# Performance work log

Measured on AMD Instinct MI355X. Metric: run time of the kernel, lower is better.

Reference implementation:

```python
import jax, jax.numpy as jnp
import numpy as np

NEG_SLOPE = 0.2  # PyG GATConv default negative_slope


def gat_layer(x, src, dst, N, W, att_src, att_dst, bias, heads, out_ch, concat):
    # x: [N, Fin]; W: [Fin, heads*out_ch]; att_*: [heads, out_ch]; bias matches output dim
    h = (x @ W).reshape(N, heads, out_ch)              # [N, H, C]
    a_src = (h * att_src).sum(-1)                      # [N, H]
    a_dst = (h * att_dst).sum(-1)                      # [N, H]
    e = jax.nn.leaky_relu(a_src[src] + a_dst[dst], NEG_SLOPE)  # [E, H]
    # segment softmax over incoming edges of each destination node
    e_max = jax.ops.segment_max(e, dst, num_segments=N)        # [N, H]
    e_exp = jnp.exp(e - e_max[dst])                             # [E, H]
    denom = jax.ops.segment_sum(e_exp, dst, num_segments=N)    # [N, H]
    alpha = e_exp / (denom[dst] + 1e-16)                        # [E, H]
    msg = alpha[:, :, None] * h[src]                            # [E, H, C]
    out = jax.ops.segment_sum(msg, dst, num_segments=N)        # [N, H, C]
    out = out.reshape(N, heads * out_ch) if concat else out.mean(axis=1)
    return out + bias


def setup_inputs() -> dict:
    key = jax.random.key(0)
    ks = jax.random.split(key, 10)
    N, E = 40000, 160000
    Fin, H1, C1 = 602, 8, 256
    H2, C2 = 1, 42
    g = lambda k, shape, fan: (jax.random.normal(k, shape, dtype=jnp.float32) * (1.0 / np.sqrt(fan)))
    return {
        "x": jax.random.normal(ks[0], (N, Fin), dtype=jnp.float32),
        "edge_index": jax.random.randint(ks[1], (2, E), 0, N, dtype=jnp.int64),
        "W1": g(ks[2], (Fin, H1 * C1), Fin),
        "att_src1": g(ks[3], (H1, C1), C1),
        "att_dst1": g(ks[4], (H1, C1), C1),
        "b1": jnp.zeros((H1 * C1,), dtype=jnp.float32),
        "W2": g(ks[5], (H1 * C1, H2 * C2), H1 * C1),
        "att_src2": g(ks[6], (H2, C2), C2),
        "att_dst2": g(ks[7], (H2, C2), C2),
        "b2": jnp.zeros((C2,), dtype=jnp.float32),
    }


def reference(x, edge_index, W1, att_src1, att_dst1, b1, W2, att_src2, att_dst2, b2):
    N = x.shape[0]
    # PyG GATConv default add_self_loops=True
    loops = jnp.arange(N, dtype=edge_index.dtype)
    src = jnp.concatenate([edge_index[0], loops])
    dst = jnp.concatenate([edge_index[1], loops])
    h = gat_layer(x, src, dst, N, W1, att_src1, att_dst1, b1, heads=8, out_ch=256, concat=True)
    h = jax.nn.relu(h)  # dropout is identity in eval mode
    h = gat_layer(h, src, dst, N, W2, att_src2, att_dst2, b2, heads=1, out_ch=42, concat=False)
    return jax.nn.log_softmax(h, axis=1)
```

## Files before the change

kernel.cpp:

```cpp
#include <hip/hip_runtime.h>
#include <hip/hip_bf16.h>

#define NN   40000
#define NE   160000
#define ETOT 200000
#define FIN  602
#define NH1  8
#define C1   256
#define F1   2048
#define C2   42
#define NEG  0.2f
#define NB   157
#define KP   608
#define MP   40064

typedef unsigned short u16;
typedef unsigned int   u32;
typedef __bf16 bf16x8 __attribute__((ext_vector_type(8)));
typedef float  f32x4  __attribute__((ext_vector_type(4)));

__device__ __forceinline__ float bfu(u16 v){ return __uint_as_float(((u32)v) << 16); }
__device__ __forceinline__ float bflo(u32 u){ return __uint_as_float(u << 16); }
__device__ __forceinline__ float bfhi(u32 u){ return __uint_as_float(u & 0xffff0000u); }
__device__ __forceinline__ u16 f2bf(float f){
  u32 u = __float_as_uint(f);
  u32 r = (u + 0x7fffu + ((u >> 16) & 1u)) >> 16;
  return (u16)r;
}

__global__ void probe_k(const u32* __restrict__ xw, const int* __restrict__ ei,
                        int* __restrict__ flags) {
  if (threadIdx.x == 0) {
    int zc = 0;
    for (int k = 0; k < 64; ++k) zc += (ei[2*k + 1] == 0) ? 1 : 0;
    flags[0] = (zc == 64) ? 1 : 0;
    int inr = 0;
    for (int k = 0; k < 64; ++k) {
      u32 low = xw[k] & 0xffffu;
      int e = (int)((low >> 7) & 0xff);
      inr += (e >= 100 && e <= 140) ? 1 : 0;
    }
    flags[1] = (inr >= 32) ? 0 : 1;
  }
}

__global__ void cvt_f32_k(const void* __restrict__ src, float* __restrict__ dst, int n,
                          const int* __restrict__ flags) {
  int i = blockIdx.x * 256 + threadIdx.x;
  if (i >= n) return;
  dst[i] = flags[1] ? ((const float*)src)[i] : bfu(((const u16*)src)[i]);
}

__global__ void xb_k(const void* __restrict__ x, u16* __restrict__ xb,
                     const int* __restrict__ flags) {
  int k = blockIdx.x * 256 + threadIdx.x;
  int row = blockIdx.y;
  if (k >= KP) return;
  u16 v = 0;
  if (row < NN && k < FIN)
    v = flags[1] ? f2bf(((const float*)x)[(size_t)row * FIN + k])
                 : ((const u16*)x)[(size_t)row * FIN + k];
  xb[(size_t)row * KP + k] = v;
}

__global__ void w1t_k(const void* __restrict__ W1, u16* __restrict__ w1t,
                      const int* __restrict__ flags) {
  int n = blockIdx.x * 256 + threadIdx.x;
  int k = blockIdx.y;
  if (n >= F1) return;
  u16 v = 0;
  if (k < FIN) v = flags[1] ? f2bf(((const float*)W1)[(size_t)k * F1 + n])
                            : ((const u16*)W1)[(size_t)k * F1 + n];
  w1t[(size_t)n * KP + k] = v;
}

__global__ void w2t_k(const void* __restrict__ W2, u16* __restrict__ w2t,
                      const int* __restrict__ flags) {
  int i = blockIdx.x * 256 + threadIdx.x;
  if (i >= 64 * F1) return;
  int c = i >> 11, k = i & (F1 - 1);
  u16 v = 0;
  if (c < C2) v = flags[1] ? f2bf(((const float*)W2)[(size_t)k * C2 + c])
                           : ((const u16*)W2)[(size_t)k * C2 + c];
  w2t[i] = v;
}

__device__ __forceinline__ void edge_sd(const int* __restrict__ ei, int e, int imode,
                                        int& s, int& d) {
  if (e < NE) {
    if (imode) { s = ei[2*e]; d = ei[2*(NE + e)]; }
    else       { s = ei[e];   d = ei[NE + e];     }
  } else { s = d = e - NE; }
}

__global__ void deg_k(const int* __restrict__ ei, int* __restrict__ deg,
                      const int* __restrict__ flags) {
  int e = blockIdx.x * 256 + threadIdx.x;
  if (e >= ETOT) return;
  int s, d; edge_sd(ei, e, flags[0], s, d);
  atomicAdd(&deg[d], 1);
}

__global__ __launch_bounds__(256) void scan1_k(const int* __restrict__ deg,
                                               int* __restrict__ tmp, int* __restrict__ bsum) {
  __shared__ int s[256];
  int b = blockIdx.x, t = threadIdx.x, i = b * 256 + t;
  int v = (i < NN) ? deg[i] : 0;
  s[t] = v; __syncthreads();
  for (int o = 1; o < 256; o <<= 1) {
    int u = (t >= o) ? s[t - o] : 0;
    __syncthreads(); s[t] += u; __syncthreads();
  }
  if (i < NN) tmp[i] = s[t];
  if (t == 255) bsum[b] = s[255];
}

__global__ __launch_bounds__(256) void scan2_k(int* __restrict__ bsum) {
  __shared__ int s[256];
  int t = threadIdx.x;
  int v = (t < NB) ? bsum[t] : 0;
  s[t] = v; __syncthreads();
  for (int o = 1; o < 256; o <<= 1) {
    int u = (t >= o) ? s[t - o] : 0;
    __syncthreads(); s[t] += u; __syncthreads();
  }
  if (t < NB) bsum[t] = s[t];
}

__global__ void scan3_k(const int* __restrict__ deg, const int* __restrict__ tmp,
                        const int* __restrict__ bsum, int* __restrict__ start, int* __restrict__ cur) {
  int i = blockIdx.x * 256 + threadIdx.x;
  if (i >= NN) return;
  int b = i >> 8;
  int off = b ? bsum[b - 1] : 0;
  int excl = tmp[i] - deg[i] + off;
  start[i] = excl; cur[i] = excl;
}

__global__ void fill_k(const int* __restrict__ ei, int* __restrict__ cur,
                       int* __restrict__ csr_src, int* __restrict__ csr_dst,
                       const int* __restrict__ flags) {
  int e = blockIdx.x * 256 + threadIdx.x;
  if (e >= ETOT) return;
  int s, d; edge_sd(ei, e, flags[0], s, d);
  int pos = atomicAdd(&cur[d], 1);
  csr_src[pos] = s; csr_dst[pos] = d;
}

__global__ __launch_bounds__(256) void gemm1b_k(const u16* __restrict__ xb,
                                                const u16* __restrict__ w1t,
                                                u16* __restrict__ h1,
                                                const float* __restrict__ as1c,
                                                const float* __restrict__ ad1c,
                                                float* __restrict__ a_s1,
                                                float* __restrict__ a_d1) {
  const int t = threadIdx.x;
  const int lane = t & 63, wid = t >> 6;
  const int wr = wid >> 1, wc = wid & 1;
  const int m0 = blockIdx.y * 128, n0 = blockIdx.x * 128;
  const int l16 = lane & 15, lk = (lane >> 4) * 8;
  f32x4 acc[4][4];
  #pragma unroll
  for (int i = 0; i < 4; ++i)
    #pragma unroll
    for (int j = 0; j < 4; ++j) acc[i][j] = (f32x4){0.f, 0.f, 0.f, 0.f};

  const u16* Ap = xb  + (size_t)(m0 + wr * 64 + l16) * KP + lk;
  const u16* Bp = w1t + (size_t)(n0 + wc * 64 + l16) * KP + lk;

  bf16x8 a[4], b[4];
  #pragma unroll
  for (int i = 0; i < 4; ++i) {
    a[i] = *(const bf16x8*)(Ap + (size_t)i * 16 * KP);
    b[i] = *(const bf16x8*)(Bp + (size_t)i * 16 * KP);
  }
  for (int k0 = 32; k0 < KP; k0 += 32) {
    bf16x8 an[4], bn[4];
    #pragma unroll
    for (int i = 0; i < 4; ++i) {
      an[i] = *(const bf16x8*)(Ap + (size_t)i * 16 * KP + k0);
      bn[i] = *(const bf16x8*)(Bp + (size_t)i * 16 * KP + k0);
    }
    #pragma unroll
    for (int mi = 0; mi < 4; ++mi)
      #pragma unroll
      for (int ni = 0; ni < 4; ++ni)
        acc[mi][ni] = __builtin_amdgcn_mfma_f32_16x16x32_bf16(a[mi], b[ni], acc[mi][ni], 0, 0, 0);
    #pragma unroll
    for (int i = 0; i < 4; ++i) { a[i] = an[i]; b[i] = bn[i]; }
  }
  #pragma unroll
  for (int mi = 0; mi < 4; ++mi)
    #pragma unroll
    for (int ni = 0; ni < 4; ++ni)
      acc[mi][ni] = __builtin_amdgcn_mfma_f32_16x16x32_bf16(a[mi], b[ni], acc[mi][ni], 0, 0, 0);

  const int h0 = n0 >> 8;
  float psrc[4][4], pdst[4][4];
  #pragma unroll
  for (int mi = 0; mi < 4; ++mi)
    #pragma unroll
    for (int r = 0; r < 4; ++r) { psrc[mi][r] = 0.f; pdst[mi][r] = 0.f; }
  #pragma unroll
  for (int ni = 0; ni < 4; ++ni) {
    int col = n0 + wc * 64 + ni * 16 + l16;
    float wsv = as1c[col], wdv = ad1c[col];
    #pragma unroll
    for (int mi = 0; mi < 4; ++mi)
      #pragma unroll
      for (int r = 0; r < 4; ++r) {
        float v = acc[mi][ni][r];
        psrc[mi][r] += v * wsv;
        pdst[mi][r] += v * wdv;
      }
  }
  #pragma unroll
  for (int o = 1; o < 16; o <<= 1) {
    #pragma unroll
    for (int mi = 0; mi < 4; ++mi)
      #pragma unroll
      for (int r = 0; r < 4; ++r) {
        psrc[mi][r] += __shfl_xor(psrc[mi][r], o, 64);
        pdst[mi][r] += __shfl_xor(pdst[mi][r], o, 64);
      }
  }
  const int lr4 = (lane >> 4) * 4;
  if (l16 == 0) {
    #pragma unroll
    for (int mi = 0; mi < 4; ++mi)
      #pragma unroll
      for (int r = 0; r < 4; ++r) {
        int row = m0 + wr * 64 + mi * 16 + lr4 + r;
        if (row < NN) {
          atomicAdd(&a_s1[row * NH1 + h0], psrc[mi][r]);
          atomicAdd(&a_d1[row * NH1 + h0], pdst[mi][r]);
        }
      }
  }

  #pragma unroll
  for (int mi = 0; mi < 4; ++mi) {
    #pragma unroll
    for (int r = 0; r < 4; ++r) {
      int row = m0 + wr * 64 + mi * 16 + lr4 + r;
      if (row < NN) {
        #pragma unroll
        for (int ni = 0; ni < 4; ++ni) {
          int col = n0 + wc * 64 + ni * 16 + l16;
          h1[(size_t)row * F1 + col] = f2bf(acc[mi][ni][r]);
        }
      }
    }
  }
}

__global__ __launch_bounds__(256) void gemm1m_k(const void* __restrict__ xv,
                                                const u16* __restrict__ w1t,
                                                u16* __restrict__ h1,
                                                const int* __restrict__ flags) {
  __shared__ u16 As[128][40];
  __shared__ u16 Bs[128][40];
  const int fm = flags[1];
  const int t = threadIdx.x;
  const int lane = t & 63, wid = t >> 6;
  const int wr = wid >> 1, wc = wid & 1;
  const int m0 = blockIdx.y * 128, n0 = blockIdx.x * 128;
  const int l16 = lane & 15, lk = (lane >> 4) * 8;
  f32x4 acc[4][4];
  #pragma unroll
  for (int i = 0; i < 4; ++i)
    #pragma unroll
    for (int j = 0; j < 4; ++j) acc[i][j] = (f32x4){0.f, 0.f, 0.f, 0.f};
  const int arow = t >> 2;
  const int akb  = (t & 3) * 8;
  for (int k0 = 0; k0 < KP; k0 += 32) {
    #pragma unroll
    for (int i = 0; i < 2; ++i) {
      int row = arow + i * 64;
      int rg = m0 + row;
      u32 d0 = 0, d1 = 0, d2 = 0, d3 = 0;
      if (rg < NN) {
        if (k0 + 32 <= FIN) {
          if (fm) {
            const float* xp = (const float*)xv + (size_t)rg * FIN + k0 + akb;
            float2 p0 = *(const float2*)(xp);
            float2 p1 = *(const float2*)(xp + 2);
            float2 p2 = *(const float2*)(xp + 4);
            float2 p3 = *(const float2*)(xp + 6);
            d0 = (u32)f2bf(p0.x) | ((u32)f2bf(p0.y) << 16);
            d1 = (u32)f2bf(p1.x) | ((u32)f2bf(p1.y) << 16);
            d2 = (u32)f2bf(p2.x) | ((u32)f2bf(p2.y) << 16);
            d3 = (u32)f2bf(p3.x) | ((u32)f2bf(p3.y) << 16);
          } else {
            const u16* xp = (const u16*)xv + (size_t)rg * FIN + k0 + akb;
            d0 = *(const u32*)(xp);
            d1 = *(const u32*)(xp + 2);
            d2 = *(const u32*)(xp + 4);
            d3 = *(const u32*)(xp + 6);
          }
        } else {
          u16 e[8];
          #pragma unroll
          for (int q = 0; q < 8; ++q) {
            int k = k0 + akb + q;
            e[q] = 0;
            if (k < FIN)
              e[q] = fm ? f2bf(((const float*)xv)[(size_t)rg * FIN + k])
                        : ((const u16*)xv)[(size_t)rg * FIN + k];
          }
          d0 = (u32)e[0] | ((u32)e[1] << 16);
          d1 = (u32)e[2] | ((u32)e[3] << 16);
          d2 = (u32)e[4] | ((u32)e[5] << 16);
          d3 = (u32)e[6] | ((u32)e[7] << 16);
        }
      }
      *(uint4*)&As[row][akb] = make_uint4(d0, d1, d2, d3);
      const u16* wp = w1t + (size_t)(n0 + row) * KP + k0 + akb;
      *(uint4*)&Bs[row][akb] = *(const uint4*)wp;
    }
    __syncthreads();
    bf16x8 bfr[4];
    #pragma unroll
    for (int ni = 0; ni < 4; ++ni)
      bfr[ni] = *(const bf16x8*)&Bs[wc * 64 + ni * 16 + l16][lk];
    #pragma unroll
    for (int mi = 0; mi < 4; ++mi) {
      bf16x8 af = *(const bf16x8*)&As[wr * 64 + mi * 16 + l16][lk];
      #pragma unroll
      for (int ni = 0; ni < 4; ++ni)
        acc[mi][ni] = __builtin_amdgcn_mfma_f32_16x16x32_bf16(af, bfr[ni], acc[mi][ni], 0, 0, 0);
    }
    __syncthreads();
  }
  const int lr4 = (lane >> 4) * 4;
  #pragma unroll
  for (int mi = 0; mi < 4; ++mi) {
    #pragma unroll
    for (int r = 0; r < 4; ++r) {
      int row = m0 + wr * 64 + mi * 16 + lr4 + r;
      if (row < NN) {
        #pragma unroll
        for (int ni = 0; ni < 4; ++ni) {
          int col = n0 + wc * 64 + ni * 16 + l16;
          h1[(size_t)row * F1 + col] = f2bf(acc[mi][ni][r]);
        }
      }
    }
  }
}

__global__ __launch_bounds__(256) void att1_k(const u16* __restrict__ h1,
                                              const float* __restrict__ as1c, const float* __restrict__ ad1c,
                                              float* __restrict__ a_s, float* __restrict__ a_d) {
  int n = blockIdx.x, t = threadIdx.x;
  int h = t >> 5, l = t & 31;
  int base = h * C1 + l * 8;
  const u16* hp = h1 + (size_t)n * F1 + base;
  uint4 v = *(const uint4*)hp;
  u32 w[4] = {v.x, v.y, v.z, v.w};
  float ss = 0.f, sd = 0.f;
  #pragma unroll
  for (int p = 0; p < 4; ++p) {
    float e0 = bflo(w[p]), e1 = bfhi(w[p]);
    ss += e0 * as1c[base + 2*p] + e1 * as1c[base + 2*p + 1];
    sd += e0 * ad1c[base + 2*p] + e1 * ad1c[base + 2*p + 1];
  }
  #pragma unroll
  for (int o = 16; o > 0; o >>= 1) {
    ss += __shfl_down(ss, o, 32);
    sd += __shfl_down(sd, o, 32);
  }
  if (l == 0) { a_s[n * NH1 + h] = ss; a_d[n * NH1 + h] = sd; }
}

__global__ __launch_bounds__(256) void gfuse_k(const int* __restrict__ start, const int* __restrict__ deg,
                                               const int* __restrict__ csr_src,
                                               const float* __restrict__ a_s1, const float* __restrict__ a_d1,
                                               const u16* __restrict__ h1, const float* __restrict__ b1c,
                                               const u16* __restrict__ w2t, float* __restrict__ h2) {
  __shared__ u16 rowsL[16 * F1];
  int t = threadIdx.x;
  int nb = blockIdx.x * 16;
  int h = t >> 5;
  int c0 = t * 8;
  float4 bA = *(const float4*)(b1c + c0);
  float4 bB = *(const float4*)(b1c + c0 + 4);
  for (int i = 0; i < 16; ++i) {
    int n = nb + i;
    int s0 = start[n], jend = s0 + deg[n];
    float ad = a_d1[n * NH1 + h];
    float a0=0.f,a1=0.f,a2=0.f,a3=0.f,a4=0.f,a5=0.f,a6=0.f,a7=0.f,den=0.f;
    int j = s0;
    for (; j + 2 <= jend; j += 2) {
      int sA = csr_src[j], sB = csr_src[j + 1];
      float vA = a_s1[sA * NH1 + h] + ad;
      float vB = a_s1[sB * NH1 + h] + ad;
      vA = vA > 0.f ? vA : NEG * vA;
      vB = vB > 0.f ? vB : NEG * vB;
      float eA = expf(vA), eB = expf(vB);
      uint4 uA = *(const uint4*)(h1 + (size_t)sA * F1 + c0);
      uint4 uB = *(const uint4*)(h1 + (size_t)sB * F1 + c0);
      den += eA + eB;
      a0 += eA * bflo(uA.x) + eB * bflo(uB.x);
      a1 += eA * bfhi(uA.x) + eB * bfhi(uB.x);
      a2 += eA * bflo(uA.y) + eB * bflo(uB.y);
      a3 += eA * bfhi(uA.y) + eB * bfhi(uB.y);
      a4 += eA * bflo(uA.z) + eB * bflo(uB.z);
      a5 += eA * bfhi(uA.z) + eB * bfhi(uB.z);
      a6 += eA * bflo(uA.w) + eB * bflo(uB.w);
      a7 += eA * bfhi(uA.w) + eB * bfhi(uB.w);
    }
    if (j < jend) {
      int sA = csr_src[j];
      float vA = a_s1[sA * NH1 + h] + ad;
      vA = vA > 0.f ? vA : NEG * vA;
      float eA = expf(vA);
      uint4 uA = *(const uint4*)(h1 + (size_t)sA * F1 + c0);
      den += eA;
      a0 += eA * bflo(uA.x); a1 += eA * bfhi(uA.x);
      a2 += eA * bflo(uA.y); a3 += eA * bfhi(uA.y);
      a4 += eA * bflo(uA.z); a5 += eA * bfhi(uA.z);
      a6 += eA * bflo(uA.w); a7 += eA * bfhi(uA.w);
    }
    float inv = 1.f / (den + 1e-16f);
    u16 o0 = f2bf(fmaxf(a0 * inv + bA.x, 0.f));
    u16 o1 = f2bf(fmaxf(a1 * inv + bA.y, 0.f));
    u16 o2 = f2bf(fmaxf(a2 * inv + bA.z, 0.f));
    u16 o3 = f2bf(fmaxf(a3 * inv + bA.w, 0.f));
    u16 o4 = f2bf(fmaxf(a4 * inv + bB.x, 0.f));
    u16 o5 = f2bf(fmaxf(a5 * inv + bB.y, 0.f));
    u16 o6 = f2bf(fmaxf(a6 * inv + bB.z, 0.f));
    u16 o7 = f2bf(fmaxf(a7 * inv + bB.w, 0.f));
    uint4 pk;
    pk.x = (u32)o0 | ((u32)o1 << 16);
    pk.y = (u32)o2 | ((u32)o3 << 16);
    pk.z = (u32)o4 | ((u32)o5 << 16);
    pk.w = (u32)o6 | ((u32)o7 << 16);
    int sw = (i & 7) << 3;
    *(uint4*)&rowsL[i * F1 + (c0 ^ sw)] = pk;
  }
  __syncthreads();
  int lane = t & 63, wid = t >> 6;
  int l16 = lane & 15, lk = (lane >> 4) * 8;
  const u16* wt = w2t + (size_t)(wid * 16 + l16) * F1;
  int sw = (l16 & 7) << 3;
  f32x4 acc2 = (f32x4){0.f, 0.f, 0.f, 0.f};
  for (int k0 = 0; k0 < F1; k0 += 32) {
    int kk = k0 + lk;
    bf16x8 af = *(const bf16x8*)&rowsL[l16 * F1 + (kk ^ sw)];
    bf16x8 bf = *(const bf16x8*)(wt + kk);
    acc2 = __builtin_amdgcn_mfma_f32_16x16x32_bf16(af, bf, acc2, 0, 0, 0);
  }
  int col = wid * 16 + l16;
  if (col < C2) {
    int mb = (lane >> 4) * 4;
    #pragma unroll
    for (int r = 0; r < 4; ++r)
      h2[(size_t)(nb + mb + r) * C2 + col] = acc2[r];
  }
}

__global__ __launch_bounds__(64) void att2_k(const float* __restrict__ h2,
                                             const float* __restrict__ as2, const float* __restrict__ ad2,
                                             float* __restrict__ a_s, float* __restrict__ a_d) {
  int n = blockIdx.x, t = threadIdx.x;
  float ss = 0.f, sd = 0.f;
  if (t < C2) {
    float v = h2[(size_t)n * C2 + t];
    ss = v * as2[t];
    sd = v * ad2[t];
  }
  #pragma unroll
  for (int o = 32; o > 0; o >>= 1) {
    ss += __shfl_down(ss, o, 64);
    sd += __shfl_down(sd, o, 64);
  }
  if (t == 0) { a_s[n] = ss; a_d[n] = sd; }
}

__global__ __launch_bounds__(64) void gath2_k(const int* __restrict__ start, const int* __restrict__ deg,
                                              const int* __restrict__ csr_src,
                                              const float* __restrict__ a_s, const float* __restrict__ a_d,
                                              const float* __restrict__ h2, const float* __restrict__ b2,
                                              void* __restrict__ outv, const int* __restrict__ flags) {
  int n = blockIdx.x, t = threadIdx.x;
  int s0 = start[n], cnt = deg[n];
  float ad = a_d[n];
  float acc = 0.f, den = 0.f;
  for (int j = s0; j < s0 + cnt; ++j) {
    int s = csr_src[j];
    float v = a_s[s] + ad;
    v = v > 0.f ? v : NEG * v;
    float e = expf(v);
    den += e;
    if (t < C2) acc += e * h2[(size_t)s * C2 + t];
  }
  float raw = (t < C2) ? acc / (den + 1e-16f) + b2[t] : -1e30f;
  float m = raw;
  #pragma unroll
  for (int o = 32; o > 0; o >>= 1) m = fmaxf(m, __shfl_down(m, o, 64));
  m = __shfl(m, 0, 64);
  float e2 = (t < C2) ? expf(raw - m) : 0.f;
  float ssum = e2;
  #pragma unroll
  for (int o = 32; o > 0; o >>= 1) ssum += __shfl_down(ssum, o, 64);
  ssum = __shfl(ssum, 0, 64);
  if (t < C2) {
    float v = raw - m - logf(ssum);
    if (flags[1]) ((float*)outv)[(size_t)n * C2 + t] = v;
    else          ((u16*) outv)[(size_t)n * C2 + t] = f2bf(v);
  }
}

extern "C" void kernel_launch(void* const* d_in, const int* in_sizes, int n_in,
                              void* d_out, int out_size, void* d_ws, size_t ws_size,
                              hipStream_t stream) {
  const void* x   = d_in[0];
  const int*  ei  = (const int*)d_in[1];
  const void* W1  = d_in[2];
  const void* as1 = d_in[3];
  const void* ad1 = d_in[4];
  const void* b1  = d_in[5];
  const void* W2  = d_in[6];
  const void* as2 = d_in[7];
  const void* ad2 = d_in[8];
  const void* b2  = d_in[9];

  char* ws = (char*)d_ws;
  u16*   h1      = (u16*)  (ws);
  float* ex1     = (float*)(ws + 163840000);
  float* h2      = (float*)(ws + 170240000);
  float* a_s1    = (float*)(ws + 176960000);
  float* a_d1    = (float*)(ws + 178240000);
  float* a_s2    = (float*)(ws + 179520000);
  float* a_d2    = (float*)(ws + 179680000);
  int*   deg     = (int*)  (ws + 179840000);
  int*   start   = (int*)  (ws + 180000000);
  int*   cur     = (int*)  (ws + 180160000);
  int*   tmp     = (int*)  (ws + 180320000);
  int*   csr_src = (int*)  (ws + 180480000);
  int*   csr_dst = (int*)  (ws + 181280000);
  int*   bsum    = (int*)  (ws + 182080000);
  u16*   w1t     = (u16*)  (ws + 182081024);
  u16*   w2t     = (u16*)  (ws + 184571392);
  float* as1c    = (float*)(ws + 184833536);
  float* ad1c    = (float*)(ws + 184841728);
  float* b1c     = (float*)(ws + 184849920);
  float* as2c    = (float*)(ws + 184858112);
  float* ad2c    = (float*)(ws + 184858368);
  float* b2c     = (float*)(ws + 184858624);
  int*   flags   = (int*)  (ws + 184858880);
  const size_t TOTAL_BASE = 184859136;
  u16*   xb      = (u16*)  (ws + TOTAL_BASE);
  const size_t TOTAL_A = TOTAL_BASE + (size_t)MP * KP * 2;
  if (ws_size < TOTAL_BASE) return;
  const bool pathA = (ws_size >= TOTAL_A);
  (void)ex1;

  probe_k<<<1, 64, 0, stream>>>((const u32*)x, ei, flags);

  cvt_f32_k<<<(F1 + 255) / 256, 256, 0, stream>>>(as1, as1c, F1, flags);
  cvt_f32_k<<<(F1 + 255) / 256, 256, 0, stream>>>(ad1, ad1c, F1, flags);
  cvt_f32_k<<<(F1 + 255) / 256, 256, 0, stream>>>(b1, b1c, F1, flags);
  cvt_f32_k<<<1, 256, 0, stream>>>(as2, as2c, C2, flags);
  cvt_f32_k<<<1, 256, 0, stream>>>(ad2, ad2c, C2, flags);
  cvt_f32_k<<<1, 256, 0, stream>>>(b2, b2c, C2, flags);
  w1t_k<<<dim3(8, KP), 256, 0, stream>>>(W1, w1t, flags);
  w2t_k<<<(64 * F1 + 255) / 256, 256, 0, stream>>>(W2, w2t, flags);

  hipMemsetAsync(deg, 0, NN * sizeof(int), stream);
  hipMemsetAsync(a_s1, 0, 2 * NN * NH1 * sizeof(float), stream);
  const int EB = (ETOT + 255) / 256;
  deg_k  <<<EB, 256, 0, stream>>>(ei, deg, flags);
  scan1_k<<<NB, 256, 0, stream>>>(deg, tmp, bsum);
  scan2_k<<<1, 256, 0, stream>>>(bsum);
  scan3_k<<<NB, 256, 0, stream>>>(deg, tmp, bsum, start, cur);
  fill_k <<<EB, 256, 0, stream>>>(ei, cur, csr_src, csr_dst, flags);

  if (pathA) {
    xb_k<<<dim3((KP + 255) / 256, MP), 256, 0, stream>>>(x, xb, flags);
    gemm1b_k<<<dim3(16, MP / 128), 256, 0, stream>>>(xb, w1t, h1, as1c, ad1c, a_s1, a_d1);
  } else {
    gemm1m_k<<<dim3(16, MP / 128), 256, 0, stream>>>(x, w1t, h1, flags);
    att1_k<<<NN, 256, 0, stream>>>(h1, as1c, ad1c, a_s1, a_d1);
  }
  gfuse_k<<<NN / 16, 256, 0, stream>>>(start, deg, csr_src, a_s1, a_d1, h1, b1c, w2t, h2);

  att2_k<<<NN, 64, 0, stream>>>(h2, as2c, ad2c, a_s2, a_d2);
  gath2_k<<<NN, 64, 0, stream>>>(start, deg, csr_src, a_s2, a_d2, h2, b2c, d_out, flags);
}
```

Baseline: 660.4 us.

## Swizzle GEMM1 block order for XCD locality and split gfuse over 512 threads

The first GEMM now runs on a 1D grid whose block index is remapped so that consecutive blocks on each of the 8 XCDs share row tiles, aiming to improve L2 reuse of A and B tiles. The fused gather+GEMM2 kernel doubles its block to 512 threads. Two groups of 256 threads each gather 8 destination nodes, and the second MFMA stage splits K in half across wave pairs with a shared-memory reduction. This raises parallelism per block and hides gather latency, at the cost of an extra barrier and fewer resident blocks per CU.

```diff
diff --git a/kernel.cpp b/kernel.cpp
--- a/kernel.cpp
+++ b/kernel.cpp
@@ -13,6 +13,7 @@
 #define NB   157
 #define KP   608
 #define MP   40064
+#define NWG1 5008
 
 typedef unsigned short u16;
 typedef unsigned int   u32;
@@ -157,7 +158,10 @@
   const int t = threadIdx.x;
   const int lane = t & 63, wid = t >> 6;
   const int wr = wid >> 1, wc = wid & 1;
-  const int m0 = blockIdx.y * 128, n0 = blockIdx.x * 128;
+  const int bid = blockIdx.x;
+  const int swz = (bid & 7) * (NWG1 / 8) + (bid >> 3);
+  const int m0 = (swz >> 4) * 128;
+  const int n0 = (swz & 15) * 128;
   const int l16 = lane & 15, lk = (lane >> 4) * 8;
   f32x4 acc[4][4];
   #pragma unroll
@@ -373,19 +377,22 @@
   if (l == 0) { a_s[n * NH1 + h] = ss; a_d[n * NH1 + h] = sd; }
 }
 
-__global__ __launch_bounds__(256) void gfuse_k(const int* __restrict__ start, const int* __restrict__ deg,
+__global__ __launch_bounds__(512) void gfuse_k(const int* __restrict__ start, const int* __restrict__ deg,
                                                const int* __restrict__ csr_src,
                                                const float* __restrict__ a_s1, const float* __restrict__ a_d1,
                                                const u16* __restrict__ h1, const float* __restrict__ b1c,
                                                const u16* __restrict__ w2t, float* __restrict__ h2) {
   __shared__ u16 rowsL[16 * F1];
+  __shared__ float pb[4][16][16];
   int t = threadIdx.x;
   int nb = blockIdx.x * 16;
-  int h = t >> 5;
-  int c0 = t * 8;
+  int sub = t & 255, grp = t >> 8;
+  int h = sub >> 5;
+  int c0 = sub * 8;
   float4 bA = *(const float4*)(b1c + c0);
   float4 bB = *(const float4*)(b1c + c0 + 4);
-  for (int i = 0; i < 16; ++i) {
+  for (int ii = 0; ii < 8; ++ii) {
+    int i = grp * 8 + ii;
     int n = nb + i;
     int s0 = start[n], jend = s0 + deg[n];
     float ad = a_d1[n * NH1 + h];
@@ -441,22 +448,31 @@
   }
   __syncthreads();
   int lane = t & 63, wid = t >> 6;
+  int g = wid & 3, kh = wid >> 2;
   int l16 = lane & 15, lk = (lane >> 4) * 8;
-  const u16* wt = w2t + (size_t)(wid * 16 + l16) * F1;
+  const u16* wt = w2t + (size_t)(g * 16 + l16) * F1;
   int sw = (l16 & 7) << 3;
   f32x4 acc2 = (f32x4){0.f, 0.f, 0.f, 0.f};
-  for (int k0 = 0; k0 < F1; k0 += 32) {
-    int kk = k0 + lk;
+  const int kbase = kh * (F1 / 2);
+  for (int k0 = 0; k0 < F1 / 2; k0 += 32) {
+    int kk = kbase + k0 + lk;
     bf16x8 af = *(const bf16x8*)&rowsL[l16 * F1 + (kk ^ sw)];
     bf16x8 bf = *(const bf16x8*)(wt + kk);
     acc2 = __builtin_amdgcn_mfma_f32_16x16x32_bf16(af, bf, acc2, 0, 0, 0);
   }
-  int col = wid * 16 + l16;
-  if (col < C2) {
-    int mb = (lane >> 4) * 4;
-    #pragma unroll
-    for (int r = 0; r < 4; ++r)
-      h2[(size_t)(nb + mb + r) * C2 + col] = acc2[r];
+  int mb = (lane >> 4) * 4;
+  if (kh == 1) {
+    #pragma unroll
+    for (int r = 0; r < 4; ++r) pb[g][mb + r][l16] = acc2[r];
+  }
+  __syncthreads();
+  if (kh == 0) {
+    int col = g * 16 + l16;
+    if (col < C2) {
+      #pragma unroll
+      for (int r = 0; r < 4; ++r)
+        h2[(size_t)(nb + mb + r) * C2 + col] = acc2[r] + pb[g][mb + r][l16];
+    }
   }
 }
 
@@ -579,12 +595,12 @@
 
   if (pathA) {
     xb_k<<<dim3((KP + 255) / 256, MP), 256, 0, stream>>>(x, xb, flags);
-    gemm1b_k<<<dim3(16, MP / 128), 256, 0, stream>>>(xb, w1t, h1, as1c, ad1c, a_s1, a_d1);
+    gemm1b_k<<<NWG1, 256, 0, stream>>>(xb, w1t, h1, as1c, ad1c, a_s1, a_d1);
   } else {
     gemm1m_k<<<dim3(16, MP / 128), 256, 0, stream>>>(x, w1t, h1, flags);
     att1_k<<<NN, 256, 0, stream>>>(h1, as1c, ad1c, a_s1, a_d1);
   }
-  gfuse_k<<<NN / 16, 256, 0, stream>>>(start, deg, csr_src, a_s1, a_d1, h1, b1c, w2t, h2);
+  gfuse_k<<<NN / 16, 512, 0, stream>>>(start, deg, csr_src, a_s1, a_d1, h1, b1c, w2t, h2);
 
   att2_k<<<NN, 64, 0, stream>>>(h2, as2c, ad2c, a_s2, a_d2);
   gath2_k<<<NN, 64, 0, stream>>>(start, deg, csr_src, a_s2, a_d2, h2, b2c, d_out, flags);
```

Result: slower. 682.1 us (+3.3%).
